# Optimization experiments

Measured on AMD Instinct MI355X. Metric: run time of the kernel, lower is better.

## Reference

```python
import jax, jax.numpy as jnp
from jax import lax
import numpy as np

B, T, D, H, OUT = 64, 1024, 256, 512, 256

def _uniform(key, shape, bound):
    return jax.random.uniform(key, shape, jnp.float32, -bound, bound)

def setup_inputs() -> dict:
    key = jax.random.key(0)
    ks = jax.random.split(key, 12)
    bnd = 1.0 / np.sqrt(H)
    inp = {
        "input": jax.random.normal(ks[0], (B, T, D), jnp.float32),
        # layer 0: input_size -> hidden_size
        "W_ih0": _uniform(ks[1], (4 * H, D), bnd),
        "W_hh0": _uniform(ks[2], (4 * H, H), bnd),
        "b_ih0": _uniform(ks[3], (4 * H,), bnd),
        "b_hh0": _uniform(ks[4], (4 * H,), bnd),
        # layer 1: hidden_size -> hidden_size
        "W_ih1": _uniform(ks[5], (4 * H, H), bnd),
        "W_hh1": _uniform(ks[6], (4 * H, H), bnd),
        "b_ih1": _uniform(ks[7], (4 * H,), bnd),
        "b_hh1": _uniform(ks[8], (4 * H,), bnd),
        # final projection
        "fc_w": _uniform(ks[9], (OUT, H), bnd),
        "fc_b": _uniform(ks[10], (OUT,), bnd),
    }
    return inp

def _lstm_layer(x_seq, W_ih, W_hh, b_ih, b_hh):
    # x_seq: [T, B, Din] -> hidden sequence [T, B, H]
    Bb = x_seq.shape[1]
    Hh = W_hh.shape[1]
    # precompute input-to-hidden projection for all timesteps (one big GEMM)
    xW = jnp.einsum("tbd,gd->tbg", x_seq, W_ih) + b_ih + b_hh  # [T, B, 4H]

    def step(carry, xw):
        h, c = carry
        gates = xw + h @ W_hh.T  # [B, 4H]
        i, f, g, o = jnp.split(gates, 4, axis=-1)
        c_new = jax.nn.sigmoid(f) * c + jax.nn.sigmoid(i) * jnp.tanh(g)
        h_new = jax.nn.sigmoid(o) * jnp.tanh(c_new)
        return (h_new, c_new), h_new

    init = (jnp.zeros((Bb, Hh), x_seq.dtype), jnp.zeros((Bb, Hh), x_seq.dtype))
    _, hs = lax.scan(step, init, xW)
    return hs  # [T, B, H]

def reference(input, W_ih0, W_hh0, b_ih0, b_hh0, W_ih1, W_hh1, b_ih1, b_hh1, fc_w, fc_b):
    x = jnp.transpose(input, (1, 0, 2))  # [T, B, D], matches input.permute(1,0,2)
    h1 = _lstm_layer(x, W_ih0, W_hh0, b_ih0, b_hh0)   # layer 0 over all timesteps
    h2 = _lstm_layer(h1, W_ih1, W_hh1, b_ih1, b_hh1)  # layer 1 consumes layer-0 outputs
    last = h2[-1]  # outs[-1].squeeze(): [B, H] (squeeze is a no-op here)
    return last @ fc_w.T + fc_b  # [B, OUT]
```

## Files before the change

kernel.cpp:

```cpp
#include <hip/hip_runtime.h>
#include <hip/hip_bf16.h>
#include <stdint.h>

typedef short short8 __attribute__((ext_vector_type(8)));
typedef float f32x4  __attribute__((ext_vector_type(4)));
typedef float fvec4  __attribute__((ext_vector_type(4)));

#define SCOPE_AGENT __HIP_MEMORY_SCOPE_AGENT
#define MFMA(a,b,c) __builtin_amdgcn_mfma_f32_16x16x32_bf16((a),(b),(c),0,0,0)

constexpr int nT = 1024, nD = 256, nH = 512, nO = 256;
constexpr int SLOT_ELEMS = 64 * 1024;
constexpr size_t SLOT_BYTES = (size_t)SLOT_ELEMS * 2;
constexpr int FPAD = 32;
constexpr size_t FLAGS_BYTES = 256 * FPAD * 4;
constexpr size_t RING_OFF = FLAGS_BYTES + 8192;
constexpr int NEG = -0x40000000;

#define K4(M)  M(0) M(1) M(2) M(3)
#define GK2(M) M(0,0) M(1,0) M(2,0) M(3,0) M(0,1) M(1,1) M(2,1) M(3,1)
#define GK4(M) GK2(M) M(0,2) M(1,2) M(2,2) M(3,2) M(0,3) M(1,3) M(2,3) M(3,3)

__device__ __forceinline__ float sigm(float x){ return 1.f/(1.f + __expf(-x)); }

__device__ __forceinline__ short8 cvt8h(const float* p){
  fvec4 a = *(const fvec4*)p;
  fvec4 b = *(const fvec4*)(p + 4);
  short8 hi;
  #pragma unroll
  for (int j = 0; j < 8; j++){
    float v = (j < 4) ? a[j] : b[j-4];
    hi[j] = (short)__bfloat16_as_ushort(__float2bfloat16(v));
  }
  return hi;
}
__device__ __forceinline__ void cvt8(const float* p, short8& hi, short8& lo){
  fvec4 a = *(const fvec4*)p;
  fvec4 b = *(const fvec4*)(p + 4);
  #pragma unroll
  for (int j = 0; j < 8; j++){
    float v = (j < 4) ? a[j] : b[j-4];
    __hip_bfloat16 h = __float2bfloat16(v);
    float r = v - __bfloat162float(h);
    hi[j] = (short)__bfloat16_as_ushort(h);
    lo[j] = (short)__bfloat16_as_ushort(__float2bfloat16(r));
  }
}
__device__ __forceinline__ unsigned pack2(float a, float b){
  return (unsigned)__bfloat16_as_ushort(__float2bfloat16(a)) |
         ((unsigned)__bfloat16_as_ushort(__float2bfloat16(b)) << 16);
}
__device__ __forceinline__ unsigned pack2lo(float a, float b){
  float ra = a - __bfloat162float(__float2bfloat16(a));
  float rb = b - __bfloat162float(__float2bfloat16(b));
  return pack2(ra, rb);
}

template<int FAST>
__device__ __forceinline__ short8 ldh(const short* p){
  if constexpr (FAST){
    return *(const short8*)p;
  } else {
    union { unsigned long long u[2]; short8 v; } r;
    const unsigned long long* q = (const unsigned long long*)p;
    r.u[0] = __hip_atomic_load(q,     __ATOMIC_RELAXED, SCOPE_AGENT);
    r.u[1] = __hip_atomic_load(q + 1, __ATOMIC_RELAXED, SCOPE_AGENT);
    return r.v;
  }
}

__device__ __forceinline__ void poll(const int* fb, int t0, int t1){
  if (threadIdx.x < 64){
    int lid = threadIdx.x;
    int tgt = (lid < 32) ? t0 : t1;
    const int* p = fb + lid * FPAD;
    int spins = 0;
    for(;;){
      int v = __hip_atomic_load(p, __ATOMIC_RELAXED, SCOPE_AGENT);
      if (__all(v >= tgt)) break;
      if (++spins > (1<<17)) break;
      if (spins > 64) __builtin_amdgcn_s_sleep(1);
    }
  }
  __syncthreads();
}

template<int FAST>
__global__ __launch_bounds__(256, 1)
__attribute__((amdgpu_waves_per_eu(1, 1)))
void lstm_kernel(
    const float* __restrict__ x,
    const float* __restrict__ Wih0, const float* __restrict__ Whh0,
    const float* __restrict__ bih0, const float* __restrict__ bhh0,
    const float* __restrict__ Wih1, const float* __restrict__ Whh1,
    const float* __restrict__ bih1, const float* __restrict__ bhh1,
    const float* __restrict__ fcw, const float* __restrict__ fcb,
    float* __restrict__ out,
    short* __restrict__ h1r, short* __restrict__ h2r,
    float* __restrict__ h2last, int* __restrict__ flags, int* __restrict__ arrive)
{
  constexpr int S1M = FAST ? 31 : 7;
  constexpr int S2M = FAST ? 31 : 3;
  constexpr int BPS = FAST ? 24 : 7;

  const int bid   = blockIdx.x;
  const int grp   = bid & 7;
  const int layer = grp & 1;
  const int bs    = grp >> 1;
  const int ns    = bid >> 3;
  const int tid   = threadIdx.x;
  const int w     = tid >> 6;
  const int l     = tid & 63;
  const int lm    = l & 15;
  const int ke    = (l >> 4) << 3;
  const int kw4   = w << 2;
  const int kw2   = w << 1;

  int* fb     = flags + (bs << 6) * FPAD;
  int* myflag = fb + ((layer << 5) + ns) * FPAD;

  __shared__ float glds[4][4][16][17];

  __builtin_amdgcn_fence(__ATOMIC_SEQ_CST, "agent");
  __syncthreads();
  if (tid == 0) __hip_atomic_fetch_add(arrive, 1, __ATOMIC_RELAXED, SCOPE_AGENT);
  if (tid < 64){
    int spins = 0;
    while (__hip_atomic_load(arrive, __ATOMIC_RELAXED, SCOPE_AGENT) < 256){
      if (++spins > (1<<20)) break;
      __builtin_amdgcn_s_sleep(1);
    }
  }
  __syncthreads();

  #define GCOL(g) ((g<<9) + (ns<<4) + lm)
  const int brow = (bs << 4) + lm;
  const int bl   = tid >> 4, jj = tid & 15;
  const int hcolbase = ns << 4;

  float c_reg = 0.f;
  float bia0, bia1, bia2, bia3;
  {
    const float* bi = layer ? bih1 : bih0;
    const float* bh = layer ? bhh1 : bhh0;
    int c0 = (ns<<4) + jj;
    bia0 = bi[c0]      + bh[c0];
    bia1 = bi[512+c0]  + bh[512+c0];
    bia2 = bi[1024+c0] + bh[1024+c0];
    bia3 = bi[1536+c0] + bh[1536+c0];
  }

  #define GWR(g) { _Pragma("unroll")                                            \
    for (int r = 0; r < 4; r++) glds[w][g][((l>>4)<<2)+r][lm] = p##g[r]; }
  #define CELLX(SLOTBASE, T, LAST)                                              \
  {                                                                             \
    GWR(0) GWR(1) GWR(2) GWR(3)                                                 \
    __syncthreads();                                                            \
    float gi = glds[0][0][bl][jj]+glds[1][0][bl][jj]+glds[2][0][bl][jj]+glds[3][0][bl][jj]+bia0; \
    float gf = glds[0][1][bl][jj]+glds[1][1][bl][jj]+glds[2][1][bl][jj]+glds[3][1][bl][jj]+bia1; \
    float gg = glds[0][2][bl][jj]+glds[1][2][bl][jj]+glds[2][2][bl][jj]+glds[3][2][bl][jj]+bia2; \
    float go = glds[0][3][bl][jj]+glds[1][3][bl][jj]+glds[2][3][bl][jj]+glds[3][3][bl][jj]+bia3; \
    float cn = sigm(gf)*c_reg + sigm(gi)*tanhf(gg);                             \
    c_reg = cn;                                                                 \
    float hn  = sigm(go)*tanhf(cn);                                             \
    float hn1 = __shfl_down(hn, 1);                                             \
    unsigned u0  = pack2(hn, hn1),  ul0 = pack2lo(hn, hn1);                     \
    unsigned u1  = __shfl_down(u0, 2), ul1 = __shfl_down(ul0, 2);               \
    if (!(jj & 3)){                                                             \
      short* p = (SLOTBASE) + bl*1024 + hcolbase + jj;                          \
      __hip_atomic_store((unsigned long long*)p,                                \
          (unsigned long long)u0 | ((unsigned long long)u1 << 32),              \
          __ATOMIC_RELAXED, SCOPE_AGENT);                                       \
      __hip_atomic_store((unsigned long long*)(p + 512),                        \
          (unsigned long long)ul0 | ((unsigned long long)ul1 << 32),            \
          __ATOMIC_RELAXED, SCOPE_AGENT);                                       \
    }                                                                           \
    if (LAST)                                                                   \
      __hip_atomic_store(h2last + (size_t)((bs<<4)+bl)*nH + hcolbase + jj, hn,  \
                         __ATOMIC_RELAXED, SCOPE_AGENT);                        \
    __syncthreads();             \
    if (tid == 0)                                                               \
      __hip_atomic_store(myflag, (T), __ATOMIC_RELAXED, SCOPE_AGENT);           \
  }

  if (layer == 0){
    #define DWX(g,i) short8 wxh##g##_##i;
    GK2(DWX)
    #define LWX(g,i) wxh##g##_##i = cvt8h(Wih0 + (size_t)GCOL(g)*nD + (kw2+i)*32 + ke);
    GK2(LWX)
    #define DWH(g,i) short8 whh##g##_##i;
    GK4(DWH)
    #define LWH(g,i) whh##g##_##i = cvt8h(Whh0 + (size_t)GCOL(g)*nH + (kw4+i)*32 + ke);
    GK4(LWH)

    f32x4 xc0={0,0,0,0}, xc1={0,0,0,0}, xc2={0,0,0,0}, xc3={0,0,0,0};
    {
      const float* xb = x + ((size_t)brow*nT)*nD + ke + kw2*32;
      short8 th0, tl0, th1, tl1;
      cvt8(xb, th0, tl0); cvt8(xb + 32, th1, tl1);
      #define XM0(g,i) xc##g = MFMA(th##i, wxh##g##_##i, xc##g);                \
                       xc##g = MFMA(tl##i, wxh##g##_##i, xc##g);
      GK2(XM0)
    }

    for (int t = 0; t < nT; t++){
      poll(fb, t-1, t-BPS);
      if constexpr (FAST)
        if ((t & 15) == 0) __builtin_amdgcn_fence(__ATOMIC_ACQUIRE, "agent");
      const short* hb = h1r + (size_t)((t+S1M)&S1M)*SLOT_ELEMS + brow*1024;
      #define HLD0(i) short8 vh##i = ldh<FAST>(hb + (kw4+i)*32 + ke);           \
                      short8 vl##i = ldh<FAST>(hb + 512 + (kw4+i)*32 + ke);
      K4(HLD0)
      f32x4 xn0={0,0,0,0}, xn1={0,0,0,0}, xn2={0,0,0,0}, xn3={0,0,0,0};
      if (t + 1 < nT){
        const float* xb = x + ((size_t)brow*nT + (t+1))*nD + ke + kw2*32;
        short8 th0, tl0, th1, tl1;
        cvt8(xb, th0, tl0); cvt8(xb + 32, th1, tl1);
        #define XMN(g,i) xn##g = MFMA(th##i, wxh##g##_##i, xn##g);              \
                         xn##g = MFMA(tl##i, wxh##g##_##i, xn##g);
        GK2(XMN)
      }
      f32x4 p0a=xc0, p1a=xc1, p2a=xc2, p3a=xc3;
      f32x4 p0b={0,0,0,0}, p1b={0,0,0,0}, p2b={0,0,0,0}, p3b={0,0,0,0};
      f32x4 p0c={0,0,0,0}, p1c={0,0,0,0}, p2c={0,0,0,0}, p3c={0,0,0,0};
      f32x4 p0d={0,0,0,0}, p1d={0,0,0,0}, p2d={0,0,0,0}, p3d={0,0,0,0};
      #define HMM0(g,i) { f32x4& d = (i==0)?p##g##a:((i==1)?p##g##b:((i==2)?p##g##c:p##g##d)); \
        d = MFMA(vh##i, whh##g##_##i, d); d = MFMA(vl##i, whh##g##_##i, d); }
      GK4(HMM0)
      f32x4 p0=(p0a+p0b)+(p0c+p0d), p1=(p1a+p1b)+(p1c+p1d);
      f32x4 p2=(p2a+p2b)+(p2c+p2d), p3=(p3a+p3b)+(p3c+p3d);
      CELLX(h1r + (size_t)(t&S1M)*SLOT_ELEMS + (bs<<4)*1024, t, 0)
      xc0 = xn0; xc1 = xn1; xc2 = xn2; xc3 = xn3;
    }
  } else {
    #define DWA(g,i) short8 ahh##g##_##i;
    GK4(DWA)
    #define LWA(g,i) ahh##g##_##i = cvt8h(Whh1 + (size_t)GCOL(g)*nH + (kw4+i)*32 + ke);
    GK4(LWA)
    #define DWB(g,i) short8 bwh##g##_##i;
    GK4(DWB)
    #define LWB(g,i) bwh##g##_##i = cvt8h(Wih1 + (size_t)GCOL(g)*nH + (kw4+i)*32 + ke);
    GK4(LWB)

    for (int t = 0; t < nT; t++){
      poll(fb, t, t-1);
      if constexpr (FAST)
        if ((t & 15) == 0) __builtin_amdgcn_fence(__ATOMIC_ACQUIRE, "agent");
      const short* h2b = h2r + (size_t)((t+S2M)&S2M)*SLOT_ELEMS + brow*1024;
      const short* h1b = h1r + (size_t)(t&S1M)*SLOT_ELEMS + brow*1024;
      #define HLD2(i) short8 u2h##i = ldh<FAST>(h2b + (kw4+i)*32 + ke);         \
                      short8 u2l##i = ldh<FAST>(h2b + 512 + (kw4+i)*32 + ke);
      K4(HLD2)
      #define HLD1(i) short8 u1h##i = ldh<FAST>(h1b + (kw4+i)*32 + ke);         \
                      short8 u1l##i = ldh<FAST>(h1b + 512 + (kw4+i)*32 + ke);
      K4(HLD1)
      f32x4 p0a={0,0,0,0}, p1a={0,0,0,0}, p2a={0,0,0,0}, p3a={0,0,0,0};
      f32x4 p0b={0,0,0,0}, p1b={0,0,0,0}, p2b={0,0,0,0}, p3b={0,0,0,0};
      f32x4 p0c={0,0,0,0}, p1c={0,0,0,0}, p2c={0,0,0,0}, p3c={0,0,0,0};
      f32x4 p0d={0,0,0,0}, p1d={0,0,0,0}, p2d={0,0,0,0}, p3d={0,0,0,0};
      #define HMM2(g,i) { f32x4& d = (i==0)?p##g##a:((i==1)?p##g##b:((i==2)?p##g##c:p##g##d)); \
        d = MFMA(u2h##i, ahh##g##_##i, d); d = MFMA(u2l##i, ahh##g##_##i, d); }
      GK4(HMM2)
      #define HMM1(g,i) { f32x4& d = (i==0)?p##g##a:((i==1)?p##g##b:((i==2)?p##g##c:p##g##d)); \
        d = MFMA(u1h##i, bwh##g##_##i, d); d = MFMA(u1l##i, bwh##g##_##i, d); }
      GK4(HMM1)
      f32x4 p0=(p0a+p0b)+(p0c+p0d), p1=(p1a+p1b)+(p1c+p1d);
      f32x4 p2=(p2a+p2b)+(p2c+p2d), p3=(p3a+p3b)+(p3c+p3d);
      CELLX(h2r + (size_t)(t&S2M)*SLOT_ELEMS + (bs<<4)*1024, t, (t == nT-1))
    }

    if (ns < 16){
      poll(fb, NEG, nT-1);
      const int orow = (bs<<4) + bl;
      const int ocol = (ns<<4) + jj;
      const unsigned long long* hq = (const unsigned long long*)(h2last + (size_t)orow*nH);
      const float* wr = fcw + (size_t)ocol*nH;
      float s0=0.f, s1=0.f, s2=0.f, s3=0.f;
      #pragma unroll 8
      for (int k = 0; k < nH; k += 8){
        union{ unsigned long long u; float f[2]; } q0,q1,q2,q3;
        q0.u = __hip_atomic_load(hq + (k>>1)    , __ATOMIC_RELAXED, SCOPE_AGENT);
        q1.u = __hip_atomic_load(hq + (k>>1) + 1, __ATOMIC_RELAXED, SCOPE_AGENT);
        q2.u = __hip_atomic_load(hq + (k>>1) + 2, __ATOMIC_RELAXED, SCOPE_AGENT);
        q3.u = __hip_atomic_load(hq + (k>>1) + 3, __ATOMIC_RELAXED, SCOPE_AGENT);
        fvec4 w0 = *(const fvec4*)(wr + k);
        fvec4 w1 = *(const fvec4*)(wr + k + 4);
        s0 += q0.f[0]*w0[0] + q0.f[1]*w0[1];
        s1 += q1.f[0]*w0[2] + q1.f[1]*w0[3];
        s2 += q2.f[0]*w1[0] + q2.f[1]*w1[1];
        s3 += q3.f[0]*w1[2] + q3.f[1]*w1[3];
      }
      out[(size_t)orow*nO + ocol] = s0 + s1 + s2 + s3 + fcb[ocol];
    }
  }
}

extern "C" void kernel_launch(void* const* d_in, const int* in_sizes, int n_in,
                              void* d_out, int out_size, void* d_ws, size_t ws_size,
                              hipStream_t stream)
{
  char* ws = (char*)d_ws;
  int* flags  = (int*)ws;
  int* arrive = (int*)(ws + FLAGS_BYTES);

  size_t need_fast = RING_OFF + 64ull*SLOT_BYTES + (size_t)64*512*4 + 4096;
  const int fast = (ws_size >= need_fast) ? 1 : 0;
  const int s1 = fast ? 32 : 8, s2 = fast ? 32 : 4;

  short* h1r = (short*)(ws + RING_OFF);
  short* h2r = h1r + (size_t)s1 * SLOT_ELEMS;
  float* h2last = (float*)(h2r + (size_t)s2 * SLOT_ELEMS);

  hipMemsetAsync(ws, 0xFF, FLAGS_BYTES, stream);
  hipMemsetAsync(ws + FLAGS_BYTES, 0, 64, stream);
  hipMemsetAsync(h1r + (size_t)(s1-1)*SLOT_ELEMS, 0, SLOT_BYTES, stream);
  hipMemsetAsync(h2r + (size_t)(s2-1)*SLOT_ELEMS, 0, SLOT_BYTES, stream);

  const float* x    = (const float*)d_in[0];
  const float* Wih0 = (const float*)d_in[1];
  const float* Whh0 = (const float*)d_in[2];
  const float* bih0 = (const float*)d_in[3];
  const float* bhh0 = (const float*)d_in[4];
  const float* Wih1 = (const float*)d_in[5];
  const float* Whh1 = (const float*)d_in[6];
  const float* bih1 = (const float*)d_in[7];
  const float* bhh1 = (const float*)d_in[8];
  const float* fcw  = (const float*)d_in[9];
  const float* fcb  = (const float*)d_in[10];
  float* out = (float*)d_out;

  if (fast)
    lstm_kernel<1><<<256, 256, 0, stream>>>(x, Wih0, Whh0, bih0, bhh0,
        Wih1, Whh1, bih1, bhh1, fcw, fcb, out, h1r, h2r, h2last, flags, arrive);
  else
    lstm_kernel<0><<<256, 256, 0, stream>>>(x, Wih0, Whh0, bih0, bhh0,
        Wih1, Whh1, bih1, bhh1, fcw, fcb, out, h1r, h2r, h2last, flags, arrive);
}
```

Measured before the change: 4.381 ms.

## Replace block-wide flag polling with per-wave arrival counters and targeted waits

Swaps the per-block timestep flag, written after a trailing __syncthreads by thread 0, for per-block counters that each wave bumps with an atomic add once its own stores have drained. Each wave now polls only the producer blocks whose h columns it actually reads, instead of the whole block waiting on all 64 flags. Layer 1 also loads h1 before waiting on its h2 peers and issues the h1 MFMAs first, and layer 0 caches a watermark for the backpressure check. The aim is to cut block-wide barrier and polling latency on the recurrent critical path. The cost is more atomic traffic, one more barrier inside the cell update, and subtler memory-ordering correctness.

Measured after the change: 5.018 ms. +14.5%, slower.

```diff
diff --git a/kernel.cpp b/kernel.cpp
--- a/kernel.cpp
+++ b/kernel.cpp
@@ -15,7 +15,6 @@
 constexpr int FPAD = 32;
 constexpr size_t FLAGS_BYTES = 256 * FPAD * 4;
 constexpr size_t RING_OFF = FLAGS_BYTES + 8192;
-constexpr int NEG = -0x40000000;
 
 #define K4(M)  M(0) M(1) M(2) M(3)
 #define GK2(M) M(0,0) M(1,0) M(2,0) M(3,0) M(0,1) M(1,1) M(2,1) M(3,1)
@@ -69,20 +68,27 @@
   }
 }
 
-__device__ __forceinline__ void poll(const int* fb, int t0, int t1){
-  if (threadIdx.x < 64){
-    int lid = threadIdx.x;
-    int tgt = (lid < 32) ? t0 : t1;
-    const int* p = fb + lid * FPAD;
-    int spins = 0;
-    for(;;){
-      int v = __hip_atomic_load(p, __ATOMIC_RELAXED, SCOPE_AGENT);
-      if (__all(v >= tgt)) break;
-      if (++spins > (1<<17)) break;
-      if (spins > 64) __builtin_amdgcn_s_sleep(1);
-    }
-  }
-  __syncthreads();
+__device__ __forceinline__ void pollN(const int* p, int cmp){
+  int spins = 0;
+  for(;;){
+    int v = __hip_atomic_load(p, __ATOMIC_RELAXED, SCOPE_AGENT);
+    if (__all(v >= cmp)) break;
+    if (++spins > (1<<17)) break;
+    if (spins > 64) __builtin_amdgcn_s_sleep(1);
+  }
+}
+__device__ __forceinline__ int wmN(const int* p, int cmp){
+  int v; int spins = 0;
+  for(;;){
+    v = __hip_atomic_load(p, __ATOMIC_RELAXED, SCOPE_AGENT);
+    if (__all(v >= cmp)) break;
+    if (++spins > (1<<17)) break;
+    if (spins > 64) __builtin_amdgcn_s_sleep(1);
+  }
+  int m = v;
+  #pragma unroll
+  for (int off = 32; off; off >>= 1) m = min(m, __shfl_xor(m, off));
+  return (m >> 2) - 1;
 }
 
 template<int FAST>
@@ -97,7 +103,7 @@
     const float* __restrict__ fcw, const float* __restrict__ fcb,
     float* __restrict__ out,
     short* __restrict__ h1r, short* __restrict__ h2r,
-    float* __restrict__ h2last, int* __restrict__ flags, int* __restrict__ arrive)
+    float* __restrict__ h2last, int* __restrict__ cnts, int* __restrict__ arrive)
 {
   constexpr int S1M = FAST ? 31 : 7;
   constexpr int S2M = FAST ? 31 : 3;
@@ -116,8 +122,8 @@
   const int kw4   = w << 2;
   const int kw2   = w << 1;
 
-  int* fb     = flags + (bs << 6) * FPAD;
-  int* myflag = fb + ((layer << 5) + ns) * FPAD;
+  int* fbc   = cnts + (bs << 6) * FPAD;
+  int* mycnt = fbc + ((layer << 5) + ns) * FPAD;
 
   __shared__ float glds[4][4][16][17];
 
@@ -154,8 +160,9 @@
     for (int r = 0; r < 4; r++) glds[w][g][((l>>4)<<2)+r][lm] = p##g[r]; }
   #define CELLX(SLOTBASE, T, LAST)                                              \
   {                                                                             \
+    __syncthreads();           \
     GWR(0) GWR(1) GWR(2) GWR(3)                                                 \
-    __syncthreads();                                                            \
+    __syncthreads();                                        \
     float gi = glds[0][0][bl][jj]+glds[1][0][bl][jj]+glds[2][0][bl][jj]+glds[3][0][bl][jj]+bia0; \
     float gf = glds[0][1][bl][jj]+glds[1][1][bl][jj]+glds[2][1][bl][jj]+glds[3][1][bl][jj]+bia1; \
     float gg = glds[0][2][bl][jj]+glds[1][2][bl][jj]+glds[2][2][bl][jj]+glds[3][2][bl][jj]+bia2; \
@@ -178,9 +185,9 @@
     if (LAST)                                                                   \
       __hip_atomic_store(h2last + (size_t)((bs<<4)+bl)*nH + hcolbase + jj, hn,  \
                          __ATOMIC_RELAXED, SCOPE_AGENT);                        \
-    __syncthreads();             \
-    if (tid == 0)                                                               \
-      __hip_atomic_store(myflag, (T), __ATOMIC_RELAXED, SCOPE_AGENT);           \
+    asm volatile("s_waitcnt vmcnt(0)" ::: "memory");         \
+    if (l == 0)                                                                 \
+      __hip_atomic_fetch_add(mycnt, 1, __ATOMIC_RELAXED, SCOPE_AGENT);          \
   }
 
   if (layer == 0){
@@ -193,6 +200,9 @@
     #define LWH(g,i) whh##g##_##i = cvt8h(Whh0 + (size_t)GCOL(g)*nH + (kw4+i)*32 + ke);
     GK4(LWH)
 
+    const int* ppeer = fbc + ((kw4 << 1) + (l & 7)) * FPAD;
+    const int* pbp   = fbc + (32 + (l & 31)) * FPAD;
+
     f32x4 xc0={0,0,0,0}, xc1={0,0,0,0}, xc2={0,0,0,0}, xc3={0,0,0,0};
     {
       const float* xb = x + ((size_t)brow*nT)*nD + ke + kw2*32;
@@ -203,10 +213,12 @@
       GK2(XM0)
     }
 
+    int wmbp = -1;
     for (int t = 0; t < nT; t++){
-      poll(fb, t-1, t-BPS);
       if constexpr (FAST)
         if ((t & 15) == 0) __builtin_amdgcn_fence(__ATOMIC_ACQUIRE, "agent");
+      if (wmbp < t - BPS) wmbp = wmN(pbp, 4*(t - BPS + 1));
+      pollN(ppeer, 4*t);
       const short* hb = h1r + (size_t)((t+S1M)&S1M)*SLOT_ELEMS + brow*1024;
       #define HLD0(i) short8 vh##i = ldh<FAST>(hb + (kw4+i)*32 + ke);           \
                       short8 vl##i = ldh<FAST>(hb + 512 + (kw4+i)*32 + ke);
@@ -242,35 +254,40 @@
     #define LWB(g,i) bwh##g##_##i = cvt8h(Wih1 + (size_t)GCOL(g)*nH + (kw4+i)*32 + ke);
     GK4(LWB)
 
+    const int* ph1 = fbc + ((kw4 << 1) + (l & 7)) * FPAD;
+    const int* ph2 = fbc + (32 + (kw4 << 1) + (l & 7)) * FPAD;
+
+    int wmh1 = -1;
     for (int t = 0; t < nT; t++){
-      poll(fb, t, t-1);
       if constexpr (FAST)
         if ((t & 15) == 0) __builtin_amdgcn_fence(__ATOMIC_ACQUIRE, "agent");
+      if (wmh1 < t) wmh1 = wmN(ph1, 4*(t + 1));
+      const short* h1b = h1r + (size_t)(t&S1M)*SLOT_ELEMS + brow*1024;
+      #define HLD1(i) short8 u1h##i = ldh<FAST>(h1b + (kw4+i)*32 + ke);         \
+                      short8 u1l##i = ldh<FAST>(h1b + 512 + (kw4+i)*32 + ke);
+      K4(HLD1)
+      pollN(ph2, 4*t);
       const short* h2b = h2r + (size_t)((t+S2M)&S2M)*SLOT_ELEMS + brow*1024;
-      const short* h1b = h1r + (size_t)(t&S1M)*SLOT_ELEMS + brow*1024;
       #define HLD2(i) short8 u2h##i = ldh<FAST>(h2b + (kw4+i)*32 + ke);         \
                       short8 u2l##i = ldh<FAST>(h2b + 512 + (kw4+i)*32 + ke);
       K4(HLD2)
-      #define HLD1(i) short8 u1h##i = ldh<FAST>(h1b + (kw4+i)*32 + ke);         \
-                      short8 u1l##i = ldh<FAST>(h1b + 512 + (kw4+i)*32 + ke);
-      K4(HLD1)
       f32x4 p0a={0,0,0,0}, p1a={0,0,0,0}, p2a={0,0,0,0}, p3a={0,0,0,0};
       f32x4 p0b={0,0,0,0}, p1b={0,0,0,0}, p2b={0,0,0,0}, p3b={0,0,0,0};
       f32x4 p0c={0,0,0,0}, p1c={0,0,0,0}, p2c={0,0,0,0}, p3c={0,0,0,0};
       f32x4 p0d={0,0,0,0}, p1d={0,0,0,0}, p2d={0,0,0,0}, p3d={0,0,0,0};
+      #define HMM1(g,i) { f32x4& d = (i==0)?p##g##a:((i==1)?p##g##b:((i==2)?p##g##c:p##g##d)); \
+        d = MFMA(u1h##i, bwh##g##_##i, d); d = MFMA(u1l##i, bwh##g##_##i, d); }
+      GK4(HMM1)
       #define HMM2(g,i) { f32x4& d = (i==0)?p##g##a:((i==1)?p##g##b:((i==2)?p##g##c:p##g##d)); \
         d = MFMA(u2h##i, ahh##g##_##i, d); d = MFMA(u2l##i, ahh##g##_##i, d); }
       GK4(HMM2)
-      #define HMM1(g,i) { f32x4& d = (i==0)?p##g##a:((i==1)?p##g##b:((i==2)?p##g##c:p##g##d)); \
-        d = MFMA(u1h##i, bwh##g##_##i, d); d = MFMA(u1l##i, bwh##g##_##i, d); }
-      GK4(HMM1)
       f32x4 p0=(p0a+p0b)+(p0c+p0d), p1=(p1a+p1b)+(p1c+p1d);
       f32x4 p2=(p2a+p2b)+(p2c+p2d), p3=(p3a+p3b)+(p3c+p3d);
       CELLX(h2r + (size_t)(t&S2M)*SLOT_ELEMS + (bs<<4)*1024, t, (t == nT-1))
     }
 
     if (ns < 16){
-      poll(fb, NEG, nT-1);
+      pollN(fbc + (32 + (l & 31)) * FPAD, 4*nT);
       const int orow = (bs<<4) + bl;
       const int ocol = (ns<<4) + jj;
       const unsigned long long* hq = (const unsigned long long*)(h2last + (size_t)orow*nH);
@@ -300,7 +317,7 @@
                               hipStream_t stream)
 {
   char* ws = (char*)d_ws;
-  int* flags  = (int*)ws;
+  int* cnts   = (int*)ws;
   int* arrive = (int*)(ws + FLAGS_BYTES);
 
   size_t need_fast = RING_OFF + 64ull*SLOT_BYTES + (size_t)64*512*4 + 4096;
@@ -311,7 +328,7 @@
   short* h2r = h1r + (size_t)s1 * SLOT_ELEMS;
   float* h2last = (float*)(h2r + (size_t)s2 * SLOT_ELEMS);
 
-  hipMemsetAsync(ws, 0xFF, FLAGS_BYTES, stream);
+  hipMemsetAsync(ws, 0, FLAGS_BYTES, stream);
   hipMemsetAsync(ws + FLAGS_BYTES, 0, 64, stream);
   hipMemsetAsync(h1r + (size_t)(s1-1)*SLOT_ELEMS, 0, SLOT_BYTES, stream);
   hipMemsetAsync(h2r + (size_t)(s2-1)*SLOT_ELEMS, 0, SLOT_BYTES, stream);
@@ -331,8 +348,8 @@
 
   if (fast)
     lstm_kernel<1><<<256, 256, 0, stream>>>(x, Wih0, Whh0, bih0, bhh0,
-        Wih1, Whh1, bih1, bhh1, fcw, fcb, out, h1r, h2r, h2last, flags, arrive);
+        Wih1, Whh1, bih1, bhh1, fcw, fcb, out, h1r, h2r, h2last, cnts, arrive);
   else
     lstm_kernel<0><<<256, 256, 0, stream>>>(x, Wih0, Whh0, bih0, bhh0,
-        Wih1, Whh1, bih1, bhh1, fcw, fcb, out, h1r, h2r, h2last, flags, arrive);
-}
+        Wih1, Whh1, bih1, bhh1, fcw, fcb, out, h1r, h2r, h2last, cnts, arrive);
+}
```
